# Kernel tuning notes

Hardware: AMD Instinct MI355X
Metric: run time of the kernel (lower is better)

The kernel has to match this reference:

```python
import jax, jax.numpy as jnp
import numpy as np
from jax import lax


def setup_inputs() -> dict:
    key = jax.random.key(0)
    k1, k2, k3 = jax.random.split(key, 3)
    B, inCh, H, Wd = 8, 64, 96, 96
    outCh, sub, kh, kw = 64, 16, 3, 3
    X = jax.random.normal(k1, (B, inCh, H, Wd), dtype=jnp.float32)
    # mimic torch Conv2d default init scale ~ 1/sqrt(fan_in)
    scale = 1.0 / np.sqrt(sub * kh * kw)
    W = jax.random.normal(k2, (outCh, sub, kh, kw), dtype=jnp.float32) * scale
    b = jax.random.normal(k3, (outCh,), dtype=jnp.float32) * scale
    return {"X": X, "W": W, "b": b}


def reference(X, W, b):
    # X: [B, inCh, H, Wd]; W: [outCh, sub, kh, kw]; b: [outCh]
    B, inCh, H, Wd = X.shape
    outCh, sub, kh, kw = W.shape
    desired = outCh + sub - 1
    reps = -(-desired // inCh)  # ceil
    # tile channels then keep first `desired` channels (matches X.repeat + slice)
    Xr = jnp.tile(X, (1, reps, 1, 1))[:, :desired]  # [B, desired, H, Wd]
    # sliding overlapping channel window: out channel o uses channels [o, o+sub)
    idx = jnp.arange(outCh)[:, None] + jnp.arange(sub)[None, :]  # [outCh, sub]
    Xw = Xr[:, idx]                         # [B, outCh, sub, H, Wd]
    Xw = Xw.reshape(B, outCh * sub, H, Wd)  # grouped-conv layout
    # grouped valid conv: group g (= out channel) contracts its own sub channels
    out = lax.conv_general_dilated(
        Xw, W, window_strides=(1, 1), padding="VALID",
        dimension_numbers=("NCHW", "OIHW", "NCHW"),
        feature_group_count=outCh,
    )  # [B, outCh, H-kh+1, Wd-kw+1]
    return out + b[None, :, None, None]
```

## Files before the change

### kernel.cpp

```cpp
#include <hip/hip_runtime.h>


typedef _Float16 f16;
typedef _Float16 f16x8 __attribute__((ext_vector_type(8)));
typedef float    f32x16 __attribute__((ext_vector_type(16)));

constexpr int IN_H = 96, IN_W = 96, OUT_H = 94, OUT_W = 94;
constexpr int NCH = 64, NOC = 64, NSUB = 16, BATCH = 8;
constexpr int NSTRIP = BATCH * 3;
constexpr int NTILES = NSTRIP * OUT_H;
constexpr size_t A_BYTES  = 2ull * 27 * 64 * 16;
constexpr size_t XN_ELEMS = (size_t)BATCH * IN_H * IN_W * NCH;
constexpr size_t XN_OFF   = A_BYTES;
constexpr size_t WS_NEEDED = XN_OFF + XN_ELEMS * 2 + 1024;

__global__ void build_a_k(const float* __restrict__ W, f16* __restrict__ Ah)
{
    const int e = blockIdx.x * 256 + threadIdx.x;
    if (e >= 2 * 27 * 64) return;
    const int lane = e & 63;
    const int r    = e >> 6;
    const int j    = r % 3;
    const int khw  = (r / 3) % 9;
    const int oh   = r / 27;
    const int cs   = oh ? (j == 0 ? 0 : j + 1) : j;
    const int kh = khw / 3, kw = khw % 3;
    const int o  = oh * 32 + (lane & 31);
    const int cb = cs * 16 + (lane >> 5) * 8;
    f16 v[8];
#pragma unroll
    for (int jj = 0; jj < 8; ++jj) {
        const int c = cb + jj;
        const int s = (c - o) & 63;
        v[jj] = (s < NSUB) ? (f16)W[((o * NSUB + s) * 3 + kh) * 3 + kw] : (f16)0.f;
    }
    *reinterpret_cast<f16x8*>(Ah + (size_t)e * 8) = *reinterpret_cast<f16x8*>(v);
}

__global__ void transpose_k(const float* __restrict__ X, f16* __restrict__ Xn)
{
    const int id = blockIdx.x;
    const int xt = id % 3;
    const int ym = id / 3;
    const int y  = ym % IN_H;
    const int b  = ym / IN_H;
    const int x  = xt * 32 + (threadIdx.x & 31);
    const int c0 = (threadIdx.x >> 5) * 8;
    const float* __restrict__ xp = X + (((size_t)(b * NCH + c0) * IN_H + y) * IN_W + x);
    f16 v[8];
#pragma unroll
    for (int i = 0; i < 8; ++i)
        v[i] = (f16)xp[(size_t)i * IN_H * IN_W];
    *reinterpret_cast<f16x8*>(Xn + ((size_t)(b * IN_H + y) * IN_W + x) * NCH + c0) =
        *reinterpret_cast<f16x8*>(v);
}

__global__ __launch_bounds__(256, 2)
void sconv_mfma(const f16* __restrict__ Ah, const f16* __restrict__ Xn,
                const float* __restrict__ Bg, float* __restrict__ Og)
{
    const int tid  = threadIdx.x;
    const int wave = tid >> 6;
    const int lane = tid & 63;
    const int oh   = wave & 1;
    const int px   = lane & 31;
    const int kg   = lane >> 5;

    const int wg = (blockIdx.x & 7) * 141 + (blockIdx.x >> 3);
    const int pairIdx = wg * 2 + (wave >> 1);
    const int strip = pairIdx / OUT_H;
    const int y     = pairIdx - strip * OUT_H;
    const int b     = strip / 3;
    const int xg    = strip - b * 3;
    const int x0    = xg * 32;

    f16x8 A[9][3];
    {
        const f16* Ab = Ah + (size_t)oh * 27 * 64 * 8;
#pragma unroll
        for (int khw = 0; khw < 9; ++khw)
#pragma unroll
            for (int j = 0; j < 3; ++j)
                A[khw][j] = *reinterpret_cast<const f16x8*>(
                    Ab + (((size_t)khw * 3 + j) * 64 + lane) * 8);
    }
    int co[3];
    co[0] = 0; co[1] = oh ? 32 : 16; co[2] = oh ? 48 : 32;

    f32x16 acc;
#pragma unroll
    for (int r = 0; r < 16; ++r)
        acc[r] = Bg[oh * 32 + (r & 3) + 8 * (r >> 2) + 4 * kg];

#pragma unroll
    for (int kh = 0; kh < 3; ++kh) {
        const f16* rp = Xn + ((size_t)(b * IN_H + (y + kh)) * IN_W) * NCH;
#pragma unroll
        for (int kw = 0; kw < 3; ++kw) {
            const f16* cp = rp + (size_t)(x0 + kw + px) * NCH + kg * 8;
            f16x8 bf[3];
#pragma unroll
            for (int j = 0; j < 3; ++j)
                bf[j] = *reinterpret_cast<const f16x8*>(cp + co[j]);
#pragma unroll
            for (int j = 0; j < 3; ++j)
                acc = __builtin_amdgcn_mfma_f32_32x32x16_f16(
                          A[kh * 3 + kw][j], bf[j], acc, 0, 0, 0);
        }
    }

    const int x = x0 + px;
    if (x < OUT_W) {
#pragma unroll
        for (int r = 0; r < 16; ++r) {
            const int o = oh * 32 + (r & 3) + 8 * (r >> 2) + 4 * kg;
            Og[(((size_t)b * NOC + o) * OUT_H + y) * OUT_W + x] = acc[r];
        }
    }
}

constexpr int TILE_X = 16, TILE_Y = 4, ROWS = TILE_Y + 2, COLS = 19;
__global__ __launch_bounds__(256, 4)
void sconv_kernel(const float* __restrict__ Xg, const float* __restrict__ Wg,
                  const float* __restrict__ Bg, float* __restrict__ Og)
{
    __shared__ float Xs[NCH][ROWS][COLS];
    const int tid = threadIdx.x, wave = tid >> 6, lane = tid & 63;
    const int x = lane & 15, y4 = lane >> 4;
    const int tx0 = blockIdx.x * TILE_X, ty0 = blockIdx.y * TILE_Y, b = blockIdx.z;
    const float* __restrict__ Xb = Xg + (size_t)b * NCH * IN_H * IN_W;
    for (int e = tid; e < NCH * ROWS * 9; e += 256) {
        const int c = e / (ROWS * 9), rm = e - c * (ROWS * 9), r = rm / 9, c2 = rm - r * 9;
        int gy = ty0 + r;      if (gy > IN_H - 1) gy = IN_H - 1;
        int gx = tx0 + 2 * c2; if (gx > IN_W - 2) gx = IN_W - 2;
        const float2 v = *reinterpret_cast<const float2*>(Xb + (c * IN_H + gy) * IN_W + gx);
        Xs[c][r][2 * c2] = v.x; Xs[c][r][2 * c2 + 1] = v.y;
    }
    __syncthreads();
    float acc[16];
#pragma unroll
    for (int i = 0; i < 16; ++i) acc[i] = 0.f;
    const int o_base = __builtin_amdgcn_readfirstlane(wave << 4);
    for (int dd = 0; dd < 31; ++dd) {
        const int c = (o_base + dd) & 63;
        float xv[3][3];
#pragma unroll
        for (int r = 0; r < 3; ++r)
#pragma unroll
            for (int kw = 0; kw < 3; ++kw) xv[r][kw] = Xs[c][y4 + r][x + kw];
#pragma unroll
        for (int jp = 0; jp < 16; ++jp)
            if ((unsigned)(dd - jp) < 16u) {
                const float* __restrict__ wp = Wg + (((o_base + jp) * NSUB) + (dd - jp)) * 9;
#pragma unroll
                for (int kh = 0; kh < 3; ++kh)
#pragma unroll
                    for (int kw = 0; kw < 3; ++kw)
                        acc[jp] = fmaf(wp[kh * 3 + kw], xv[kh][kw], acc[jp]);
            }
    }
    const int y = ty0 + y4, xo = tx0 + x;
    if (y < OUT_H && xo < OUT_W)
#pragma unroll
        for (int jp = 0; jp < 16; ++jp) {
            const int o = o_base + jp;
            Og[(((size_t)b * NOC + o) * OUT_H + y) * OUT_W + xo] = acc[jp] + Bg[o];
        }
}

extern "C" void kernel_launch(void* const* d_in, const int* in_sizes, int n_in,
                              void* d_out, int out_size, void* d_ws, size_t ws_size,
                              hipStream_t stream)
{
    const float* X = (const float*)d_in[0];
    const float* W = (const float*)d_in[1];
    const float* B = (const float*)d_in[2];
    float* O = (float*)d_out;

    if (ws_size < WS_NEEDED) {
        dim3 grid((OUT_W + TILE_X - 1) / TILE_X, (OUT_H + TILE_Y - 1) / TILE_Y, BATCH);
        sconv_kernel<<<grid, 256, 0, stream>>>(X, W, B, O);
        return;
    }

    f16* Ah = (f16*)d_ws;
    f16* Xn = (f16*)((char*)d_ws + XN_OFF);

    build_a_k<<<14, 256, 0, stream>>>(W, Ah);
    transpose_k<<<BATCH * IN_H * 3, 256, 0, stream>>>(X, Xn);
    sconv_mfma<<<NTILES / 2, 256, 0, stream>>>(Ah, Xn, B, O);
}
```

Baseline: 100.1 us.

## Fuse NCHW-to-NHWC fp16 transpose into MFMA conv via swizzled LDS tile

Removes the separate transpose kernel and its global fp16 intermediate buffer. Each 512-thread block now loads a 6-row by 36-column fp32 input halo from NCHW, converts it to fp16, and writes it into LDS in a channel-last layout with an XOR swizzle to avoid bank conflicts. The MFMA waves then read their B operands from LDS instead of global memory. This cuts a kernel launch and a full round-trip of the input through HBM. In exchange, halo rows are loaded redundantly across blocks and the global reads are strided per channel.

```diff
diff --git a/kernel.cpp b/kernel.cpp
--- a/kernel.cpp
+++ b/kernel.cpp
@@ -7,12 +7,13 @@
 
 constexpr int IN_H = 96, IN_W = 96, OUT_H = 94, OUT_W = 94;
 constexpr int NCH = 64, NOC = 64, NSUB = 16, BATCH = 8;
-constexpr int NSTRIP = BATCH * 3;
-constexpr int NTILES = NSTRIP * OUT_H;
-constexpr size_t A_BYTES  = 2ull * 27 * 64 * 16;
-constexpr size_t XN_ELEMS = (size_t)BATCH * IN_H * IN_W * NCH;
-constexpr size_t XN_OFF   = A_BYTES;
-constexpr size_t WS_NEEDED = XN_OFF + XN_ELEMS * 2 + 1024;
+constexpr int TILE_Y = 4;
+constexpr int SROWS  = TILE_Y + 2;
+constexpr int SXP    = 36;
+constexpr size_t A_BYTES   = 2ull * 27 * 64 * 16;
+constexpr size_t WS_NEEDED = A_BYTES + 256;
+
+__device__ __forceinline__ int imin(int a, int b) { return a < b ? a : b; }
 
 __global__ void build_a_k(const float* __restrict__ W, f16* __restrict__ Ah)
 {
@@ -37,42 +38,56 @@
     *reinterpret_cast<f16x8*>(Ah + (size_t)e * 8) = *reinterpret_cast<f16x8*>(v);
 }
 
-__global__ void transpose_k(const float* __restrict__ X, f16* __restrict__ Xn)
-{
-    const int id = blockIdx.x;
-    const int xt = id % 3;
-    const int ym = id / 3;
-    const int y  = ym % IN_H;
-    const int b  = ym / IN_H;
-    const int x  = xt * 32 + (threadIdx.x & 31);
-    const int c0 = (threadIdx.x >> 5) * 8;
-    const float* __restrict__ xp = X + (((size_t)(b * NCH + c0) * IN_H + y) * IN_W + x);
-    f16 v[8];
-#pragma unroll
-    for (int i = 0; i < 8; ++i)
-        v[i] = (f16)xp[(size_t)i * IN_H * IN_W];
-    *reinterpret_cast<f16x8*>(Xn + ((size_t)(b * IN_H + y) * IN_W + x) * NCH + c0) =
-        *reinterpret_cast<f16x8*>(v);
-}
-
-__global__ __launch_bounds__(256, 2)
-void sconv_mfma(const f16* __restrict__ Ah, const f16* __restrict__ Xn,
-                const float* __restrict__ Bg, float* __restrict__ Og)
-{
+__global__ __launch_bounds__(512, 2)
+void sconv_fused(const float* __restrict__ Xg, const f16* __restrict__ Ah,
+                 const float* __restrict__ Bg, float* __restrict__ Og)
+{
+    __shared__ __attribute__((aligned(16))) unsigned char lds[SROWS * SXP * 128];
+
     const int tid  = threadIdx.x;
     const int wave = tid >> 6;
     const int lane = tid & 63;
-    const int oh   = wave & 1;
-    const int px   = lane & 31;
-    const int kg   = lane >> 5;
-
-    const int wg = (blockIdx.x & 7) * 141 + (blockIdx.x >> 3);
-    const int pairIdx = wg * 2 + (wave >> 1);
-    const int strip = pairIdx / OUT_H;
-    const int y     = pairIdx - strip * OUT_H;
-    const int b     = strip / 3;
-    const int xg    = strip - b * 3;
-    const int x0    = xg * 32;
+
+    const int x0 = blockIdx.x * 32;
+    const int y0 = blockIdx.y * TILE_Y;
+    const int b  = blockIdx.z;
+
+    const float* __restrict__ Xb = Xg + (size_t)b * NCH * IN_H * IN_W;
+
+    {
+        const int xh = tid & 31;
+        const int u  = tid >> 5;
+        const int cg = u & 7;
+        const int rb = u >> 3;
+#pragma unroll
+        for (int rr = 0; rr < 3; ++rr) {
+            const int row = rb * 3 + rr;
+            const int gy  = imin(y0 + row, IN_H - 1);
+#pragma unroll
+            for (int ci = 0; ci < 8; ++ci) {
+                const int c = cg * 8 + ci;
+                const float* __restrict__ p = Xb + ((size_t)c * IN_H + gy) * IN_W;
+                const float f = p[imin(x0 + xh, IN_W - 1)];
+                *reinterpret_cast<f16*>(lds + (((row * SXP + xh) << 7) +
+                    ((cg ^ (xh & 7)) << 4) + (ci << 1))) = (f16)f;
+                if (xh < 4) {
+                    const int x2 = 32 + xh;
+                    const float f2 = p[imin(x0 + x2, IN_W - 1)];
+                    *reinterpret_cast<f16*>(lds + (((row * SXP + x2) << 7) +
+                        ((cg ^ (x2 & 7)) << 4) + (ci << 1))) = (f16)f2;
+                }
+            }
+        }
+    }
+    __syncthreads();
+
+    const int oh = wave & 1;
+    const int yy = wave >> 1;
+    const int y  = y0 + yy;
+    if (y >= OUT_H) return;
+
+    const int px = lane & 31;
+    const int kg = lane >> 5;
 
     f16x8 A[9][3];
     {
@@ -84,8 +99,8 @@
                 A[khw][j] = *reinterpret_cast<const f16x8*>(
                     Ab + (((size_t)khw * 3 + j) * 64 + lane) * 8);
     }
-    int co[3];
-    co[0] = 0; co[1] = oh ? 32 : 16; co[2] = oh ? 48 : 32;
+    int cog[3];
+    cog[0] = 0; cog[1] = oh ? 4 : 2; cog[2] = oh ? 6 : 4;
 
     f32x16 acc;
 #pragma unroll
@@ -94,14 +109,16 @@
 
 #pragma unroll
     for (int kh = 0; kh < 3; ++kh) {
-        const f16* rp = Xn + ((size_t)(b * IN_H + (y + kh)) * IN_W) * NCH;
 #pragma unroll
         for (int kw = 0; kw < 3; ++kw) {
-            const f16* cp = rp + (size_t)(x0 + kw + px) * NCH + kg * 8;
+            const int xloc = px + kw;
+            const int base = ((yy + kh) * SXP + xloc) << 7;
+            const int sx   = xloc & 7;
             f16x8 bf[3];
 #pragma unroll
             for (int j = 0; j < 3; ++j)
-                bf[j] = *reinterpret_cast<const f16x8*>(cp + co[j]);
+                bf[j] = *reinterpret_cast<const f16x8*>(
+                    lds + base + (((cog[j] + kg) ^ sx) << 4));
 #pragma unroll
             for (int j = 0; j < 3; ++j)
                 acc = __builtin_amdgcn_mfma_f32_32x32x16_f16(
@@ -119,18 +136,18 @@
     }
 }
 
-constexpr int TILE_X = 16, TILE_Y = 4, ROWS = TILE_Y + 2, COLS = 19;
+constexpr int TILE_Xf = 16, TILE_Yf = 4, ROWSf = TILE_Yf + 2, COLSf = 19;
 __global__ __launch_bounds__(256, 4)
 void sconv_kernel(const float* __restrict__ Xg, const float* __restrict__ Wg,
                   const float* __restrict__ Bg, float* __restrict__ Og)
 {
-    __shared__ float Xs[NCH][ROWS][COLS];
+    __shared__ float Xs[NCH][ROWSf][COLSf];
     const int tid = threadIdx.x, wave = tid >> 6, lane = tid & 63;
     const int x = lane & 15, y4 = lane >> 4;
-    const int tx0 = blockIdx.x * TILE_X, ty0 = blockIdx.y * TILE_Y, b = blockIdx.z;
+    const int tx0 = blockIdx.x * TILE_Xf, ty0 = blockIdx.y * TILE_Yf, b = blockIdx.z;
     const float* __restrict__ Xb = Xg + (size_t)b * NCH * IN_H * IN_W;
-    for (int e = tid; e < NCH * ROWS * 9; e += 256) {
-        const int c = e / (ROWS * 9), rm = e - c * (ROWS * 9), r = rm / 9, c2 = rm - r * 9;
+    for (int e = tid; e < NCH * ROWSf * 9; e += 256) {
+        const int c = e / (ROWSf * 9), rm = e - c * (ROWSf * 9), r = rm / 9, c2 = rm - r * 9;
         int gy = ty0 + r;      if (gy > IN_H - 1) gy = IN_H - 1;
         int gx = tx0 + 2 * c2; if (gx > IN_W - 2) gx = IN_W - 2;
         const float2 v = *reinterpret_cast<const float2*>(Xb + (c * IN_H + gy) * IN_W + gx);
@@ -178,15 +195,13 @@
     float* O = (float*)d_out;
 
     if (ws_size < WS_NEEDED) {
-        dim3 grid((OUT_W + TILE_X - 1) / TILE_X, (OUT_H + TILE_Y - 1) / TILE_Y, BATCH);
+        dim3 grid((OUT_W + TILE_Xf - 1) / TILE_Xf, (OUT_H + TILE_Yf - 1) / TILE_Yf, BATCH);
         sconv_kernel<<<grid, 256, 0, stream>>>(X, W, B, O);
         return;
     }
 
     f16* Ah = (f16*)d_ws;
-    f16* Xn = (f16*)((char*)d_ws + XN_OFF);
-
     build_a_k<<<14, 256, 0, stream>>>(W, Ah);
-    transpose_k<<<BATCH * IN_H * 3, 256, 0, stream>>>(X, Xn);
-    sconv_mfma<<<NTILES / 2, 256, 0, stream>>>(Ah, Xn, B, O);
-}
+    dim3 grid(3, (OUT_H + TILE_Y - 1) / TILE_Y, BATCH);
+    sconv_fused<<<grid, 512, 0, stream>>>(X, Ah, B, O);
+}
```

After: 92.05 us. 8.0% less time.
